# Performance work log

Measured on AMD Instinct MI355X. Metric: run time of the kernel, lower is better.

## Reference

```python
import jax, jax.numpy as jnp
import numpy as np

HEADS = 16
KV_HEADS = 4
DIM_HEAD = 128
DIM = 2048
ROPE_BASE = 10000.0


def rotate_half(t):
    t1, t2 = jnp.split(t, 2, axis=-1)
    return jnp.concatenate((-t2, t1), axis=-1)


def apply_rotary(t, cos, sin):
    # t: [b, h, n, d]; cos/sin: [n, d]
    return t * cos + rotate_half(t) * sin


def setup_inputs() -> dict:
    key = jax.random.key(0)
    ks = jax.random.split(key, 6)
    b, n = 4, 1024
    s = 1.0 / np.sqrt(DIM)
    x = jax.random.normal(ks[0], (b, n, DIM), dtype=jnp.float32)
    Wq = jax.random.normal(ks[1], (DIM, HEADS * DIM_HEAD), dtype=jnp.float32) * s
    Wk = jax.random.normal(ks[2], (DIM, KV_HEADS * DIM_HEAD), dtype=jnp.float32) * s
    Wv = jax.random.normal(ks[3], (DIM, KV_HEADS * DIM_HEAD), dtype=jnp.float32) * s
    Wo = jax.random.normal(ks[4], (HEADS * DIM_HEAD, DIM), dtype=jnp.float32) * s
    head_scale = 1.0 + 0.02 * jax.random.normal(ks[5], (1, HEADS, 1, 1), dtype=jnp.float32)
    return {"x": x, "Wq": Wq, "Wk": Wk, "Wv": Wv, "Wo": Wo, "head_scale": head_scale}


def reference(x, Wq, Wk, Wv, Wo, head_scale):
    b, n, _ = x.shape
    # projections
    q = (x @ Wq).reshape(b, n, HEADS, DIM_HEAD).transpose(0, 2, 1, 3)      # b h n d
    k = (x @ Wk).reshape(b, n, KV_HEADS, DIM_HEAD).transpose(0, 2, 1, 3)   # b kv n d
    v = (x @ Wv).reshape(b, n, KV_HEADS, DIM_HEAD).transpose(0, 2, 1, 3)
    # rotary embeddings
    inv_freq = 1.0 / (ROPE_BASE ** (jnp.arange(0, DIM_HEAD, 2, dtype=jnp.float32) / DIM_HEAD))
    freqs = jnp.arange(n, dtype=jnp.float32)[:, None] * inv_freq[None, :]  # n, d/2
    emb = jnp.concatenate((freqs, freqs), axis=-1)                          # n, d
    cos, sin = jnp.cos(emb), jnp.sin(emb)
    q = apply_rotary(q, cos, sin)
    k = apply_rotary(k, cos, sin)
    # GQA: expand kv heads to query heads
    rep = HEADS // KV_HEADS
    k = jnp.repeat(k, rep, axis=1)
    v = jnp.repeat(v, rep, axis=1)
    # attention with causal mask
    scale = 1.0 / jnp.sqrt(jnp.array(DIM_HEAD, dtype=x.dtype))
    scores = jnp.einsum('bhid,bhjd->bhij', q, k) * scale
    causal = jnp.tril(jnp.ones((n, n), dtype=bool))
    scores = jnp.where(causal, scores, jnp.finfo(scores.dtype).min)
    attn = jax.nn.softmax(scores, axis=-1)
    out = jnp.einsum('bhij,bhjd->bhid', attn, v)
    out = out * head_scale                                                  # learned per-head scale
    out = out.transpose(0, 2, 1, 3).reshape(b, n, HEADS * DIM_HEAD)
    return out @ Wo
```

## Files before the change

### kernel.cpp

```cpp
#include <hip/hip_runtime.h>

typedef __attribute__((ext_vector_type(8))) short short8;
typedef __attribute__((ext_vector_type(8), may_alias)) short short8a;
typedef __attribute__((ext_vector_type(4))) short short4a_ __attribute__((may_alias));
typedef __attribute__((ext_vector_type(2), may_alias)) short short2a;
typedef __attribute__((ext_vector_type(4))) float float4_;
typedef __attribute__((ext_vector_type(4), may_alias)) float float4a;
typedef __attribute__((ext_vector_type(2), may_alias)) float float2a;

__device__ __forceinline__ float b2f(short h) {
  unsigned int u = ((unsigned int)(unsigned short)h) << 16;
  return __builtin_bit_cast(float, u);
}
__device__ __forceinline__ short f2b(float f) {
  unsigned int u = __builtin_bit_cast(unsigned int, f);
  u += 0x7fffu + ((u >> 16) & 1u);
  return (short)(unsigned short)(u >> 16);
}

#define GLOBAL_AS __attribute__((address_space(1)))
#define LDS_AS    __attribute__((address_space(3)))
__device__ __forceinline__ void async_copy16(void* lds, const void* g) {
  __builtin_amdgcn_global_load_lds((GLOBAL_AS const void*)g, (LDS_AS void*)lds, 16, 0, 0);
}

__global__ __launch_bounds__(256) void prep(const float* __restrict__ x,
                                            const float* __restrict__ Wq,
                                            const float* __restrict__ Wk,
                                            const float* __restrict__ Wv,
                                            const float* __restrict__ Wo,
                                            short* __restrict__ xb,
                                            short* __restrict__ wqkvt,
                                            short* __restrict__ wot,
                                            float* __restrict__ rtab) {
  __shared__ float tile[64][65];
  int bid = blockIdx.x;
  if (bid < 1536) {
    int k0 = (bid & 31) * 64, n0 = (bid >> 5) * 64;
    for (int idx = threadIdx.x; idx < 4096; idx += 256) {
      int r = idx >> 6, cc = idx & 63;
      int n = n0 + cc;
      float v;
      if (n < 2048)      v = Wq[(size_t)(k0 + r) * 2048 + n] * 0.08838834764831845f;
      else if (n < 2560) v = Wk[(size_t)(k0 + r) * 512 + (n - 2048)];
      else               v = Wv[(size_t)(k0 + r) * 512 + (n - 2560)];
      tile[r][cc] = v;
    }
    __syncthreads();
    for (int idx = threadIdx.x; idx < 4096; idx += 256) {
      int r = idx >> 6, cc = idx & 63;
      wqkvt[(size_t)(n0 + r) * 2048 + k0 + cc] = f2b(tile[cc][r]);
    }
  } else if (bid < 2560) {
    int t = bid - 1536;
    int k0 = (t & 31) * 64, n0 = (t >> 5) * 64;
    for (int idx = threadIdx.x; idx < 4096; idx += 256) {
      int r = idx >> 6, cc = idx & 63;
      tile[r][cc] = Wo[(size_t)(k0 + r) * 2048 + n0 + cc];
    }
    __syncthreads();
    for (int idx = threadIdx.x; idx < 4096; idx += 256) {
      int r = idx >> 6, cc = idx & 63;
      wot[(size_t)(n0 + r) * 2048 + k0 + cc] = f2b(tile[cc][r]);
    }
  } else if (bid < 10752) {
    int i = (bid - 2560) * 256 + threadIdx.x;
    float4a v = ((const float4a*)x)[i];
    short4a_ o;
    o.x = f2b(v.x); o.y = f2b(v.y); o.z = f2b(v.z); o.w = f2b(v.w);
    ((short4a_*)xb)[i] = o;
  } else {
    int idx = (bid - 10752) * 256 + threadIdx.x;
    int pos = idx >> 6, i = idx & 63;
    float inv = exp2f((float)i * -0.20762050593478f);
    float s, c;
    sincosf((float)pos * inv, &s, &c);
    float2a cs; cs.x = c; cs.y = s;
    ((float2a*)rtab)[idx] = cs;
  }
}

template <int MODE>
__global__ __launch_bounds__(256, 2)
void gemm_bt(const short* __restrict__ A, const short* __restrict__ B,
             void* __restrict__ Cv, const float* __restrict__ rtab, int M, int N, int K) {
  __shared__ alignas(16) short lsm[MODE == 1 ? 16896 : 16384];
  short* lA = lsm;
  short* lB = lsm + 8192;
  const int tid = threadIdx.x;
  const int wave = tid >> 6, lane = tid & 63;
  const int quad = lane >> 4, l16 = lane & 15;
  const int m0 = blockIdx.x * 128, n0 = blockIdx.y * 128;
  const int wm = (wave >> 1) * 64, wn = (wave & 1) * 64;
  float4_ acc[4][4];
#pragma unroll
  for (int i = 0; i < 4; i++)
#pragma unroll
    for (int j = 0; j < 4; j++) acc[i][j] = (float4_){0.f, 0.f, 0.f, 0.f};
  const int nK = K >> 6;
  const int srow = lane >> 3, slot = lane & 7;
  for (int kt = 0; kt < nK; ++kt) {
    __syncthreads();
#pragma unroll
    for (int cth = 0; cth < 4; ++cth) {
      int rb = wave * 32 + cth * 8;
      int r = rb + srow;
      int c = slot ^ (r & 7);
      async_copy16(&lA[rb * 64], A + (size_t)(m0 + r) * K + kt * 64 + c * 8);
      async_copy16(&lB[rb * 64], B + (size_t)(n0 + r) * K + kt * 64 + c * 8);
    }
    __syncthreads();
#pragma unroll
    for (int kc = 0; kc < 2; ++kc) {
      short8 af[4], bf[4];
      int cch = kc * 4 + quad;
#pragma unroll
      for (int mt = 0; mt < 4; ++mt) {
        int ar = wm + mt * 16 + l16;
        af[mt] = *(const short8a*)&lA[ar * 64 + (cch ^ (ar & 7)) * 8];
      }
#pragma unroll
      for (int nt = 0; nt < 4; ++nt) {
        int br = wn + nt * 16 + l16;
        bf[nt] = *(const short8a*)&lB[br * 64 + (cch ^ (br & 7)) * 8];
      }
#pragma unroll
      for (int mt = 0; mt < 4; ++mt)
#pragma unroll
        for (int nt = 0; nt < 4; ++nt)
          acc[mt][nt] = __builtin_amdgcn_mfma_f32_16x16x32_bf16(af[mt], bf[nt], acc[mt][nt], 0, 0, 0);
    }
  }
  if (MODE == 1 && n0 < 2560) {
    __syncthreads();
    short* lC = lsm;
#pragma unroll
    for (int mt = 0; mt < 4; ++mt)
#pragma unroll
      for (int nt = 0; nt < 4; ++nt)
#pragma unroll
        for (int r = 0; r < 4; r++)
          lC[(wm + mt * 16 + quad * 4 + r) * 132 + wn + nt * 16 + l16] = f2b(acc[mt][nt][r]);
    __syncthreads();
    short* Cb = (short*)Cv;
    const int posBase = m0 & 1023;
#pragma unroll
    for (int it = 0; it < 16; ++it) {
      int idx = it * 256 + tid;
      int row = idx >> 5;
      int c2 = (idx & 31) * 2;
      short2a t1 = *(const short2a*)&lC[row * 132 + c2];
      short2a t2 = *(const short2a*)&lC[row * 132 + c2 + 64];
      float t1a = b2f(t1.x), t1b = b2f(t1.y);
      float t2a = b2f(t2.x), t2b = b2f(t2.y);
      float4a tv = *(const float4a*)&rtab[((size_t)(posBase + row) * 64 + c2) * 2];
      short2a o1, o2;
      o1.x = f2b(t1a * tv.x - t2a * tv.y); o1.y = f2b(t1b * tv.z - t2b * tv.w);
      o2.x = f2b(t2a * tv.x + t1a * tv.y); o2.y = f2b(t2b * tv.z + t1b * tv.w);
      size_t base = (size_t)(m0 + row) * N + n0;
      *(short2a*)&Cb[base + c2] = o1;
      *(short2a*)&Cb[base + c2 + 64] = o2;
    }
  } else {
#pragma unroll
    for (int mt = 0; mt < 4; ++mt)
#pragma unroll
      for (int nt = 0; nt < 4; ++nt) {
        int row = m0 + wm + mt * 16 + quad * 4;
        int col = n0 + wn + nt * 16 + l16;
        float4_ v = acc[mt][nt];
        if (MODE == 1) {
          short* Cb = (short*)Cv;
#pragma unroll
          for (int r = 0; r < 4; r++) Cb[(size_t)(row + r) * N + col] = f2b(v[r]);
        } else {
          float* Cf = (float*)Cv;
#pragma unroll
          for (int r = 0; r < 4; r++) Cf[(size_t)(row + r) * N + col] = v[r];
        }
      }
  }
}

__global__ __launch_bounds__(256) void vt_build(const short* __restrict__ qkv, short* __restrict__ vt) {
  __shared__ short tile[128][65];
  int bkv = blockIdx.x, n0 = blockIdx.y * 64;
  int b = bkv >> 2, kv = bkv & 3;
  const short* src = qkv + (size_t)(b * 1024) * 3072 + 2560 + kv * 128;
#pragma unroll
  for (int it = 0; it < 4; ++it) {
    int n = it * 16 + (threadIdx.x >> 4), ch = threadIdx.x & 15;
    short8a v = *(const short8a*)(src + (size_t)(n0 + n) * 3072 + ch * 8);
#pragma unroll
    for (int j = 0; j < 8; ++j) tile[ch * 8 + j][n] = v[j];
  }
  __syncthreads();
#pragma unroll
  for (int it = 0; it < 4; ++it) {
    int idx = it * 256 + threadIdx.x;
    int d = idx >> 3, ch = idx & 7;
    short8a v;
#pragma unroll
    for (int j = 0; j < 8; ++j) v[j] = tile[d][ch * 8 + j];
    *(short8a*)(vt + (size_t)(bkv * 128 + d) * 1024 + n0 + ch * 8) = v;
  }
}

__global__ __launch_bounds__(256, 2)
void flash(const short* __restrict__ qkv, const short* __restrict__ vt,
           const float* __restrict__ head_scale, short* __restrict__ attn) {
  __shared__ alignas(16) short lK[64 * 128];
  __shared__ alignas(16) short lV[128 * 64];
  __shared__ alignas(16) short lP[4][32 * 72];
  const int tid = threadIdx.x, wave = tid >> 6, lane = tid & 63;
  const int quad = lane >> 4, l16 = lane & 15;
  const int bh = blockIdx.x, b = bh >> 4, h = bh & 15, kv = h >> 2;
  const int qt = 7 - blockIdx.y;
  const int base_w = qt * 128 + wave * 32;
  short8 qf[2][4];
#pragma unroll
  for (int g = 0; g < 2; g++) {
    int qrow = base_w + g * 16 + l16;
    const short* qp = qkv + (size_t)(b * 1024 + qrow) * 3072 + h * 128;
#pragma unroll
    for (int kc = 0; kc < 4; kc++) qf[g][kc] = *(const short8a*)(qp + kc * 32 + quad * 8);
  }
  float4_ O[2][8];
#pragma unroll
  for (int g = 0; g < 2; g++)
#pragma unroll
    for (int i = 0; i < 8; i++) O[g][i] = (float4_){0.f, 0.f, 0.f, 0.f};
  float rsacc[2][4] = {{0.f, 0.f, 0.f, 0.f}, {0.f, 0.f, 0.f, 0.f}};
  const size_t kbase = (size_t)(b * 1024) * 3072 + 2048 + kv * 128;
  const size_t vbase = (size_t)((b * 4 + kv) * 128) * 1024;
  const int slot16 = lane & 15, rr4 = lane >> 4;
  const int slot8 = lane & 7, dr8 = lane >> 3;
  const int nkt = 2 * qt + 2;
  for (int kt = 0; kt < nkt; ++kt) {
    __syncthreads();
#pragma unroll
    for (int cc = 0; cc < 4; ++cc) {
      int rb = wave * 16 + cc * 4;
      int r = rb + rr4;
      int c = slot16 ^ (r & 15);
      async_copy16(&lK[rb * 128], qkv + kbase + (size_t)(kt * 64 + r) * 3072 + c * 8);
    }
#pragma unroll
    for (int cc = 0; cc < 4; ++cc) {
      int db = wave * 32 + cc * 8;
      int d = db + dr8;
      int c = slot8 ^ (d & 7);
      async_copy16(&lV[db * 64], vt + vbase + (size_t)d * 1024 + kt * 64 + c * 8);
    }
    __syncthreads();
    if (kt * 64 > base_w + 31) continue;
    float4_ S[2][4];
#pragma unroll
    for (int st = 0; st < 4; ++st) {
      float4_ s0 = (float4_){0.f, 0.f, 0.f, 0.f}, s1 = s0;
      int kr = st * 16 + l16;
#pragma unroll
      for (int kc = 0; kc < 4; ++kc) {
        int c = kc * 4 + quad;
        short8 kf = *(const short8a*)&lK[kr * 128 + (c ^ (kr & 15)) * 8];
        s0 = __builtin_amdgcn_mfma_f32_16x16x32_bf16(qf[0][kc], kf, s0, 0, 0, 0);
        s1 = __builtin_amdgcn_mfma_f32_16x16x32_bf16(qf[1][kc], kf, s1, 0, 0, 0);
      }
      S[0][st] = s0; S[1][st] = s1;
    }
#pragma unroll
    for (int g = 0; g < 2; g++) {
      int gbase = base_w + g * 16;
      if (kt * 64 + 63 > gbase) {
#pragma unroll
        for (int st = 0; st < 4; ++st)
#pragma unroll
          for (int r = 0; r < 4; r++)
            if (kt * 64 + st * 16 + l16 > gbase + quad * 4 + r) S[g][st][r] = -1e30f;
      }
#pragma unroll
      for (int st = 0; st < 4; ++st)
#pragma unroll
        for (int r = 0; r < 4; r++) {
          float pv = __expf(S[g][st][r]);
          rsacc[g][r] += pv;
          lP[wave][(g * 16 + quad * 4 + r) * 72 + st * 16 + l16] = f2b(pv);
        }
    }
    short8 pf[2][2];
#pragma unroll
    for (int g = 0; g < 2; g++)
#pragma unroll
      for (int kc2 = 0; kc2 < 2; kc2++)
        pf[g][kc2] = *(const short8a*)&lP[wave][(g * 16 + l16) * 72 + kc2 * 32 + quad * 8];
#pragma unroll
    for (int dt = 0; dt < 8; ++dt) {
      int d = dt * 16 + l16;
#pragma unroll
      for (int kc2 = 0; kc2 < 2; kc2++) {
        int c = kc2 * 4 + quad;
        short8 vf = *(const short8a*)&lV[d * 64 + (c ^ (d & 7)) * 8];
        O[0][dt] = __builtin_amdgcn_mfma_f32_16x16x32_bf16(pf[0][kc2], vf, O[0][dt], 0, 0, 0);
        O[1][dt] = __builtin_amdgcn_mfma_f32_16x16x32_bf16(pf[1][kc2], vf, O[1][dt], 0, 0, 0);
      }
    }
  }
  float hs = head_scale[h];
#pragma unroll
  for (int g = 0; g < 2; g++) {
    float l_i[4];
#pragma unroll
    for (int r = 0; r < 4; r++) {
      float rs = rsacc[g][r];
#pragma unroll
      for (int off = 8; off; off >>= 1) rs += __shfl_xor(rs, off, 64);
      l_i[r] = rs;
    }
    int qrow = base_w + g * 16 + quad * 4;
#pragma unroll
    for (int dt = 0; dt < 8; ++dt) {
      int col = h * 128 + dt * 16 + l16;
#pragma unroll
      for (int r = 0; r < 4; r++) {
        float o = O[g][dt][r] * (hs / l_i[r]);
        attn[(size_t)(b * 1024 + qrow + r) * 2048 + col] = f2b(o);
      }
    }
  }
}

extern "C" void kernel_launch(void* const* d_in, const int* in_sizes, int n_in,
                              void* d_out, int out_size, void* d_ws, size_t ws_size,
                              hipStream_t stream) {
  const float* x  = (const float*)d_in[0];
  const float* Wq = (const float*)d_in[1];
  const float* Wk = (const float*)d_in[2];
  const float* Wv = (const float*)d_in[3];
  const float* Wo = (const float*)d_in[4];
  const float* hs = (const float*)d_in[5];
  float* out = (float*)d_out;
  char* ws = (char*)d_ws;
  short* xb    = (short*)(ws);
  short* wqkvt = (short*)(ws + 16777216);
  short* wot   = (short*)(ws + 29360128);
  short* qkv   = (short*)(ws + 37748736);
  short* vt    = (short*)(ws + 62914560);
  float* rtab  = (float*)(ws + 62914560);
  short* attn  = xb;

  prep<<<11008, 256, 0, stream>>>(x, Wq, Wk, Wv, Wo, xb, wqkvt, wot, rtab);
  gemm_bt<1><<<dim3(32, 24), 256, 0, stream>>>(xb, wqkvt, (void*)qkv, rtab, 4096, 3072, 2048);
  vt_build<<<dim3(16, 16), 256, 0, stream>>>(qkv, vt);
  flash<<<dim3(64, 8), 256, 0, stream>>>(qkv, vt, hs, attn);
  gemm_bt<0><<<dim3(32, 16), 256, 0, stream>>>(attn, wot, (void*)out, nullptr, 4096, 2048, 2048);
}
```

Baseline: 253.6 us.

## Fuse V transpose into QKV GEMM epilogue and drop vt_build kernel

The QKV projection epilogue now transposes V tiles through shared memory and writes the transposed V layout directly, removing the separate vt_build kernel and its re-read of V. RoPE table loads are hoisted before the LDS staging barrier to overlap latency. The rope table is relocated into the unused tail of the output buffer. This adds register pressure from 16 held float4 values and strided LDS reads in the transpose.

```diff
diff --git a/kernel.cpp b/kernel.cpp
--- a/kernel.cpp
+++ b/kernel.cpp
@@ -83,7 +83,8 @@
 template <int MODE>
 __global__ __launch_bounds__(256, 2)
 void gemm_bt(const short* __restrict__ A, const short* __restrict__ B,
-             void* __restrict__ Cv, const float* __restrict__ rtab, int M, int N, int K) {
+             void* __restrict__ Cv, const float* __restrict__ rtab,
+             short* __restrict__ vt, int M, int N, int K) {
   __shared__ alignas(16) short lsm[MODE == 1 ? 16896 : 16384];
   short* lA = lsm;
   short* lB = lsm + 8192;
@@ -131,9 +132,20 @@
           acc[mt][nt] = __builtin_amdgcn_mfma_f32_16x16x32_bf16(af[mt], bf[nt], acc[mt][nt], 0, 0, 0);
     }
   }
-  if (MODE == 1 && n0 < 2560) {
+  if (MODE == 1) {
+    const bool isRope = (n0 < 2560);
     __syncthreads();
     short* lC = lsm;
+    const int posBase = m0 & 1023;
+    float4a tv[16];
+    if (isRope) {
+#pragma unroll
+      for (int it = 0; it < 16; ++it) {
+        int idx = it * 256 + tid;
+        int row = idx >> 5, c2 = (idx & 31) * 2;
+        tv[it] = *(const float4a*)&rtab[((size_t)(posBase + row) * 64 + c2) * 2];
+      }
+    }
 #pragma unroll
     for (int mt = 0; mt < 4; ++mt)
 #pragma unroll
@@ -142,24 +154,36 @@
         for (int r = 0; r < 4; r++)
           lC[(wm + mt * 16 + quad * 4 + r) * 132 + wn + nt * 16 + l16] = f2b(acc[mt][nt][r]);
     __syncthreads();
-    short* Cb = (short*)Cv;
-    const int posBase = m0 & 1023;
-#pragma unroll
-    for (int it = 0; it < 16; ++it) {
-      int idx = it * 256 + tid;
-      int row = idx >> 5;
-      int c2 = (idx & 31) * 2;
-      short2a t1 = *(const short2a*)&lC[row * 132 + c2];
-      short2a t2 = *(const short2a*)&lC[row * 132 + c2 + 64];
-      float t1a = b2f(t1.x), t1b = b2f(t1.y);
-      float t2a = b2f(t2.x), t2b = b2f(t2.y);
-      float4a tv = *(const float4a*)&rtab[((size_t)(posBase + row) * 64 + c2) * 2];
-      short2a o1, o2;
-      o1.x = f2b(t1a * tv.x - t2a * tv.y); o1.y = f2b(t1b * tv.z - t2b * tv.w);
-      o2.x = f2b(t2a * tv.x + t1a * tv.y); o2.y = f2b(t2b * tv.z + t1b * tv.w);
-      size_t base = (size_t)(m0 + row) * N + n0;
-      *(short2a*)&Cb[base + c2] = o1;
-      *(short2a*)&Cb[base + c2 + 64] = o2;
+    if (isRope) {
+      short* Cb = (short*)Cv;
+#pragma unroll
+      for (int it = 0; it < 16; ++it) {
+        int idx = it * 256 + tid;
+        int row = idx >> 5;
+        int c2 = (idx & 31) * 2;
+        short2a t1 = *(const short2a*)&lC[row * 132 + c2];
+        short2a t2 = *(const short2a*)&lC[row * 132 + c2 + 64];
+        float t1a = b2f(t1.x), t1b = b2f(t1.y);
+        float t2a = b2f(t2.x), t2b = b2f(t2.y);
+        float4a t = tv[it];
+        short2a o1, o2;
+        o1.x = f2b(t1a * t.x - t2a * t.y); o1.y = f2b(t1b * t.z - t2b * t.w);
+        o2.x = f2b(t2a * t.x + t1a * t.y); o2.y = f2b(t2b * t.z + t1b * t.w);
+        size_t base = (size_t)(m0 + row) * N + n0;
+        *(short2a*)&Cb[base + c2] = o1;
+        *(short2a*)&Cb[base + c2 + 64] = o2;
+      }
+    } else {
+      const int bkv = (m0 >> 10) * 4 + ((n0 - 2560) >> 7);
+#pragma unroll
+      for (int it = 0; it < 8; ++it) {
+        int idx = it * 256 + tid;
+        int d = idx >> 4, jc = idx & 15;
+        short8 v;
+#pragma unroll
+        for (int k = 0; k < 8; ++k) v[k] = lC[(jc * 8 + k) * 132 + d];
+        *(short8a*)&vt[((size_t)(bkv * 128 + d)) * 1024 + posBase + jc * 8] = v;
+      }
     }
   } else {
 #pragma unroll
@@ -169,40 +193,10 @@
         int row = m0 + wm + mt * 16 + quad * 4;
         int col = n0 + wn + nt * 16 + l16;
         float4_ v = acc[mt][nt];
-        if (MODE == 1) {
-          short* Cb = (short*)Cv;
-#pragma unroll
-          for (int r = 0; r < 4; r++) Cb[(size_t)(row + r) * N + col] = f2b(v[r]);
-        } else {
-          float* Cf = (float*)Cv;
-#pragma unroll
-          for (int r = 0; r < 4; r++) Cf[(size_t)(row + r) * N + col] = v[r];
-        }
-      }
-  }
-}
-
-__global__ __launch_bounds__(256) void vt_build(const short* __restrict__ qkv, short* __restrict__ vt) {
-  __shared__ short tile[128][65];
-  int bkv = blockIdx.x, n0 = blockIdx.y * 64;
-  int b = bkv >> 2, kv = bkv & 3;
-  const short* src = qkv + (size_t)(b * 1024) * 3072 + 2560 + kv * 128;
-#pragma unroll
-  for (int it = 0; it < 4; ++it) {
-    int n = it * 16 + (threadIdx.x >> 4), ch = threadIdx.x & 15;
-    short8a v = *(const short8a*)(src + (size_t)(n0 + n) * 3072 + ch * 8);
-#pragma unroll
-    for (int j = 0; j < 8; ++j) tile[ch * 8 + j][n] = v[j];
-  }
-  __syncthreads();
-#pragma unroll
-  for (int it = 0; it < 4; ++it) {
-    int idx = it * 256 + threadIdx.x;
-    int d = idx >> 3, ch = idx & 7;
-    short8a v;
-#pragma unroll
-    for (int j = 0; j < 8; ++j) v[j] = tile[d][ch * 8 + j];
-    *(short8a*)(vt + (size_t)(bkv * 128 + d) * 1024 + n0 + ch * 8) = v;
+        float* Cf = (float*)Cv;
+#pragma unroll
+        for (int r = 0; r < 4; r++) Cf[(size_t)(row + r) * N + col] = v[r];
+      }
   }
 }
 
@@ -345,12 +339,11 @@
   short* wot   = (short*)(ws + 29360128);
   short* qkv   = (short*)(ws + 37748736);
   short* vt    = (short*)(ws + 62914560);
-  float* rtab  = (float*)(ws + 62914560);
   short* attn  = xb;
+  float* rtab  = out + 8257536;
 
   prep<<<11008, 256, 0, stream>>>(x, Wq, Wk, Wv, Wo, xb, wqkvt, wot, rtab);
-  gemm_bt<1><<<dim3(32, 24), 256, 0, stream>>>(xb, wqkvt, (void*)qkv, rtab, 4096, 3072, 2048);
-  vt_build<<<dim3(16, 16), 256, 0, stream>>>(qkv, vt);
+  gemm_bt<1><<<dim3(32, 24), 256, 0, stream>>>(xb, wqkvt, (void*)qkv, rtab, vt, 4096, 3072, 2048);
   flash<<<dim3(64, 8), 256, 0, stream>>>(qkv, vt, hs, attn);
-  gemm_bt<0><<<dim3(32, 16), 256, 0, stream>>>(attn, wot, (void*)out, nullptr, 4096, 2048, 2048);
-}
+  gemm_bt<0><<<dim3(32, 16), 256, 0, stream>>>(attn, wot, (void*)out, nullptr, nullptr, 4096, 2048, 2048);
+}
```

New measurement: 249.3 us. About the same (-1.7%).
